# Performance work log

Hardware: AMD Instinct MI355X
Metric: run time of the kernel (lower is better)

The kernel has to match this reference:

```python
import jax, jax.numpy as jnp
import numpy as np

N_NODES = 50000
N_EDGES = 1600000
IN_DIM = 128
HEADS = 8
OUT_C = 16  # per-head channels; HEADS*OUT_C == IN_DIM -> residual active
NEG_SLOPE = 0.2
BN_EPS = 1e-5


def setup_inputs() -> dict:
    key = jax.random.key(0)
    ks = jax.random.split(key, 8)
    x = jax.random.normal(ks[0], (N_NODES, IN_DIM), dtype=jnp.float32)
    edge_index = jax.random.randint(ks[1], (2, N_EDGES), 0, N_NODES, dtype=jnp.int64)
    # GATConv params (PyG: shared lin for src/dst on single-tensor input)
    W = jax.random.normal(ks[2], (IN_DIM, HEADS * OUT_C), dtype=jnp.float32) / np.sqrt(IN_DIM)
    att_src = jax.random.normal(ks[3], (HEADS, OUT_C), dtype=jnp.float32) / np.sqrt(OUT_C)
    att_dst = jax.random.normal(ks[4], (HEADS, OUT_C), dtype=jnp.float32) / np.sqrt(OUT_C)
    bias = jnp.zeros((HEADS * OUT_C,), dtype=jnp.float32)
    # BatchNorm1d affine params
    gamma = jnp.ones((HEADS * OUT_C,), dtype=jnp.float32)
    beta = jnp.zeros((HEADS * OUT_C,), dtype=jnp.float32)
    return {"x": x, "edge_index": edge_index, "W": W, "att_src": att_src,
            "att_dst": att_dst, "bias": bias, "gamma": gamma, "beta": beta}


def reference(x, edge_index, W, att_src, att_dst, bias, gamma, beta):
    N = x.shape[0]
    H, C = att_src.shape
    src, dst = edge_index[0], edge_index[1]

    xl = (x @ W).reshape(N, H, C)                      # [N,H,C]
    a_src = jnp.sum(xl * att_src[None], axis=-1)       # [N,H]
    a_dst = jnp.sum(xl * att_dst[None], axis=-1)       # [N,H]

    e = jax.nn.leaky_relu(a_src[src] + a_dst[dst], NEG_SLOPE)  # [E,H]
    # segment softmax over incoming edges of each dst node
    m = jax.ops.segment_max(e, dst, num_segments=N)    # [N,H], -inf for empty
    m = jnp.where(jnp.isfinite(m), m, 0.0)
    ex = jnp.exp(e - m[dst])                           # [E,H]
    denom = jax.ops.segment_sum(ex, dst, num_segments=N)
    alpha = ex / (denom[dst] + 1e-16)                  # [E,H]

    out = jax.ops.segment_sum(alpha[:, :, None] * xl[src], dst, num_segments=N)  # [N,H,C]
    h = out.reshape(N, H * C) + bias

    # BatchNorm1d (training mode: batch statistics, biased variance)
    mean = jnp.mean(h, axis=0)
    var = jnp.mean((h - mean) ** 2, axis=0)
    h = (h - mean) * jax.lax.rsqrt(var + BN_EPS) * gamma + beta

    h = jax.nn.relu(h)
    return x + h  # residual (in_dim == H*C)
```

## Files before the change

kernel.cpp:

```cpp
#include <hip/hip_runtime.h>
#include <hip/hip_fp16.h>
#include <math.h>

#define N_NODES 50000
#define N_EDGES 1600000
#define DIM 128
#define HEADS 8
#define NEG_SLOPE 0.2f
#define BN_EPS 1e-5f

typedef _Float16 f16x8 __attribute__((ext_vector_type(8)));
typedef float f32x4 __attribute__((ext_vector_type(4)));

__global__ void k_wprep(const float* __restrict__ W, __half* __restrict__ Wh) {
    const int tid = blockIdx.x * 256 + threadIdx.x;
    const int g = tid >> 6;
    const int lane = tid & 63;
    const int nt = g >> 2, kt = g & 3;
    const int q = lane >> 4, n = lane & 15;
    #pragma unroll
    for (int j = 0; j < 8; ++j)
        Wh[(size_t)(g * 64 + lane) * 8 + j] =
            __float2half(W[(kt * 32 + q * 8 + j) * DIM + nt * 16 + n]);
}

__global__ __launch_bounds__(256) void k_lin(const float* __restrict__ x,
                      const __half* __restrict__ Wh, const float* __restrict__ att_s,
                      const float* __restrict__ att_d, __half* __restrict__ xlh,
                      float* __restrict__ a_src, float* __restrict__ a_dst) {
    const int wave = threadIdx.x >> 6;
    const int lane = threadIdx.x & 63;
    const int q = lane >> 4, n = lane & 15;
    const int nb = (blockIdx.x * 4 + wave) * 16;

    const int rowA = min(nb + n, N_NODES - 1);
    const float* xr = x + (size_t)rowA * DIM;
    f16x8 a[4];
    #pragma unroll
    for (int kt = 0; kt < 4; ++kt) {
        const float4 p0 = *(const float4*)(xr + kt * 32 + q * 8);
        const float4 p1 = *(const float4*)(xr + kt * 32 + q * 8 + 4);
        a[kt][0] = (_Float16)p0.x; a[kt][1] = (_Float16)p0.y;
        a[kt][2] = (_Float16)p0.z; a[kt][3] = (_Float16)p0.w;
        a[kt][4] = (_Float16)p1.x; a[kt][5] = (_Float16)p1.y;
        a[kt][6] = (_Float16)p1.z; a[kt][7] = (_Float16)p1.w;
    }

    f32x4 acc[8];
    #pragma unroll
    for (int nt = 0; nt < 8; ++nt) acc[nt] = (f32x4){0.f, 0.f, 0.f, 0.f};

    const f16x8* wb = (const f16x8*)Wh;
    #pragma unroll
    for (int nt = 0; nt < 8; ++nt) {
        #pragma unroll
        for (int kt = 0; kt < 4; ++kt) {
            const f16x8 b = wb[(nt * 4 + kt) * 64 + lane];
            acc[nt] = __builtin_amdgcn_mfma_f32_16x16x32_f16(a[kt], b, acc[nt], 0, 0, 0);
        }
    }

    const int r0 = nb + q * 4;
    #pragma unroll
    for (int nt = 0; nt < 8; ++nt) {
        const float as = att_s[nt * 16 + n];
        const float ad = att_d[nt * 16 + n];
        #pragma unroll
        for (int r = 0; r < 4; ++r) {
            const int row = r0 + r;
            const float v = acc[nt][r];
            float s = v * as;
            float d = v * ad;
            #pragma unroll
            for (int off = 8; off; off >>= 1) {
                s += __shfl_xor(s, off, 16);
                d += __shfl_xor(d, off, 16);
            }
            if (row < N_NODES) {
                xlh[(size_t)row * DIM + nt * 16 + n] = __float2half(v);
                if (n == 0) {
                    a_src[row * HEADS + nt] = s;
                    a_dst[row * HEADS + nt] = d;
                }
            }
        }
    }
}

#define SCAN_B 256
#define NBUCK 196
#define SEGCAP 12288
#define CHUNK 8192
#define NB_A ((N_EDGES + CHUNK - 1) / CHUNK)

__global__ __launch_bounds__(256) void k_binA(const int* __restrict__ ei,
                                              int* __restrict__ bcur,
                                              unsigned int* __restrict__ pairs) {
    __shared__ int hist[NBUCK], excl[NBUCK], gbase[NBUCK], cnt2[NBUCK];
    __shared__ int sc[SCAN_B];
    __shared__ unsigned int buf[CHUNK];
    const int t = threadIdx.x;
    const int base = blockIdx.x * CHUNK;
    const int cnt = min(CHUNK, N_EDGES - base);

    for (int j = t; j < NBUCK; j += 256) { hist[j] = 0; cnt2[j] = 0; }
    __syncthreads();
    for (int i = t; i < cnt; i += 256)
        atomicAdd(&hist[ei[N_EDGES + base + i] >> 8], 1);
    __syncthreads();
    sc[t] = (t < NBUCK) ? hist[t] : 0;
    __syncthreads();
    for (int d = 1; d < SCAN_B; d <<= 1) {
        const int xo = (t >= d) ? sc[t - d] : 0;
        __syncthreads();
        sc[t] += xo;
        __syncthreads();
    }
    if (t < NBUCK) {
        excl[t] = sc[t] - hist[t];
        gbase[t] = t * SEGCAP + atomicAdd(&bcur[t], hist[t]);
    }
    __syncthreads();
    for (int i = t; i < cnt; i += 256) {
        const int s = ei[base + i];
        const int d = ei[N_EDGES + base + i];
        const int b = d >> 8;
        const int r = atomicAdd(&cnt2[b], 1);
        buf[excl[b] + r] = (unsigned int)s | ((unsigned int)(d & 255) << 16)
                         | ((unsigned int)b << 24);
    }
    __syncthreads();
    for (int i = t; i < cnt; i += 256) {
        const unsigned int u = buf[i];
        const int b = u >> 24;
        pairs[gbase[b] + (i - excl[b])] = u & 0xFFFFFF;
    }
}

__global__ __launch_bounds__(512) void k_binB(const unsigned int* __restrict__ pairs,
                                              const int* __restrict__ bcur,
                                              unsigned short* __restrict__ csr,
                                              int2* __restrict__ nrange) {
    __shared__ int hist[256], excl[256], cnt2[256];
    __shared__ unsigned short out[SEGCAP];
    const int t = threadIdx.x;
    const int b = blockIdx.x;
    const int lo = b * SEGCAP;
    const int cnt = bcur[b];

    if (t < 256) { hist[t] = 0; cnt2[t] = 0; }
    __syncthreads();
    for (int i = t; i < cnt; i += 512)
        atomicAdd(&hist[pairs[lo + i] >> 16], 1);
    __syncthreads();
    if (t < 256) excl[t] = hist[t];
    __syncthreads();
    for (int d = 1; d < 256; d <<= 1) {
        int xo = 0;
        if (t < 256 && t >= d) xo = excl[t - d];
        __syncthreads();
        if (t < 256) excl[t] += xo;
        __syncthreads();
    }
    if (t < 256) excl[t] -= hist[t];
    __syncthreads();
    for (int i = t; i < cnt; i += 512) {
        const unsigned int u = pairs[lo + i];
        const int dl = u >> 16;
        const int r = atomicAdd(&cnt2[dl], 1);
        out[excl[dl] + r] = (unsigned short)(u & 0xFFFF);
    }
    __syncthreads();
    for (int i = t; i < cnt; i += 512)
        csr[2 * lo + i] = out[i];
    if (t < 256) {
        const int node = (b << 8) + t;
        if (node < N_NODES) {
            int2 rg;
            rg.x = 2 * lo + excl[t];
            rg.y = rg.x + hist[t];
            nrange[node] = rg;
        }
    }
}

__global__ void k_aggr2(const int2* __restrict__ nrange, const unsigned short* __restrict__ csr,
                        const float* __restrict__ a_src, const float* __restrict__ a_dst,
                        const __half* __restrict__ xlh, float* __restrict__ y) {
    const int d = blockIdx.x * 4 + (threadIdx.x >> 6);
    const int lane = threadIdx.x & 63;
    const int c2 = lane << 1;
    const int h = lane >> 3;
    const int2 rg = nrange[d];
    const int lo = rg.x, hi = rg.y;
    const float ad = a_dst[d * HEADS + h];
    float acc0 = 0.f, acc1 = 0.f, dsum = 0.f;
    int i = lo;
    for (; i + 8 <= hi; i += 8) {
        int s[8];
        float e[8];
        __half2 xv[8];
        #pragma unroll
        for (int j = 0; j < 8; ++j) s[j] = csr[i + j];
        #pragma unroll
        for (int j = 0; j < 8; ++j) e[j] = a_src[s[j] * HEADS + h] + ad;
        #pragma unroll
        for (int j = 0; j < 8; ++j)
            xv[j] = *(const __half2*)(xlh + (size_t)s[j] * DIM + c2);
        #pragma unroll
        for (int j = 0; j < 8; ++j) {
            const float w = __expf(fmaxf(e[j], NEG_SLOPE * e[j]));
            const float2 f = __half22float2(xv[j]);
            acc0 = fmaf(w, f.x, acc0);
            acc1 = fmaf(w, f.y, acc1);
            dsum += w;
        }
    }
    for (; i < hi; ++i) {
        const int s = csr[i];
        const float e = a_src[s * HEADS + h] + ad;
        const __half2 xv = *(const __half2*)(xlh + (size_t)s * DIM + c2);
        const float w = __expf(fmaxf(e, NEG_SLOPE * e));
        const float2 f = __half22float2(xv);
        acc0 = fmaf(w, f.x, acc0); acc1 = fmaf(w, f.y, acc1); dsum += w;
    }
    const float inv = 1.f / (dsum + 1e-16f);
    float2 o; o.x = acc0 * inv; o.y = acc1 * inv;
    *(float2*)(y + (size_t)d * DIM + c2) = o;
}

__global__ void k_stats(const float* __restrict__ y, const float* __restrict__ bias,
                        float* __restrict__ sums, float* __restrict__ sumsq) {
    const int c = threadIdx.x;
    const float b = bias[c];
    float s = 0.f, ss = 0.f;
    for (int n = blockIdx.x; n < N_NODES; n += gridDim.x) {
        const float h = y[n * DIM + c] + b;
        s += h;
        ss += h * h;
    }
    atomicAdd(sums + c, s);
    atomicAdd(sumsq + c, ss);
}

__global__ void k_statfin(const float* __restrict__ sums, const float* __restrict__ sumsq,
                          const float* __restrict__ gamma, const float* __restrict__ beta,
                          const float* __restrict__ bias, float* __restrict__ scale,
                          float* __restrict__ shift) {
    const int c = threadIdx.x;
    const float inv_n = 1.f / (float)N_NODES;
    const float mean = sums[c] * inv_n;
    const float var = sumsq[c] * inv_n - mean * mean;
    const float sc = rsqrtf(var + BN_EPS) * gamma[c];
    scale[c] = sc;
    shift[c] = beta[c] + (bias[c] - mean) * sc;
}

__global__ void k_final(float* __restrict__ y, const float* __restrict__ x,
                        const float* __restrict__ scale, const float* __restrict__ shift) {
    const int q = blockIdx.x * blockDim.x + threadIdx.x;
    const int cq = q & (DIM / 4 - 1);
    float4 v = ((const float4*)y)[q];
    const float4 xv = ((const float4*)x)[q];
    const float4 sc = ((const float4*)scale)[cq];
    const float4 sh = ((const float4*)shift)[cq];
    v.x = xv.x + fmaxf(v.x * sc.x + sh.x, 0.f);
    v.y = xv.y + fmaxf(v.y * sc.y + sh.y, 0.f);
    v.z = xv.z + fmaxf(v.z * sc.z + sh.z, 0.f);
    v.w = xv.w + fmaxf(v.w * sc.w + sh.w, 0.f);
    ((float4*)y)[q] = v;
}

extern "C" void kernel_launch(void* const* d_in, const int* in_sizes, int n_in,
                              void* d_out, int out_size, void* d_ws, size_t ws_size,
                              hipStream_t stream) {
    const float* x     = (const float*)d_in[0];
    const int*   ei    = (const int*)  d_in[1];
    const float* W     = (const float*)d_in[2];
    const float* att_s = (const float*)d_in[3];
    const float* att_d = (const float*)d_in[4];
    const float* bias  = (const float*)d_in[5];
    const float* gamma = (const float*)d_in[6];
    const float* beta  = (const float*)d_in[7];
    float* y = (float*)d_out;

    __half* xlh  = (__half*)d_ws;
    float* a_src = (float*)(xlh + (size_t)N_NODES * DIM);
    float* a_dst = a_src + (size_t)N_NODES * HEADS;
    float* sums  = a_dst + (size_t)N_NODES * HEADS;
    float* sumsq = sums  + DIM;
    float* scale = sumsq + DIM;
    float* shift = scale + DIM;
    int*   bcur  = (int*)(shift + DIM);
    int2*  nrange = (int2*)(bcur + 256);
    __half* Wh   = (__half*)(nrange + N_NODES);
    unsigned int* pairs = (unsigned int*)(Wh + 16384);
    unsigned short* csr = (unsigned short*)pairs;

    hipMemsetAsync(sums, 0, (4 * DIM + 256) * sizeof(float), stream);

    k_wprep<<<8, 256, 0, stream>>>(W, Wh);
    k_lin<<<(N_NODES + 63) / 64, 256, 0, stream>>>(x, Wh, att_s, att_d, xlh, a_src, a_dst);
    k_binA<<<NB_A, 256, 0, stream>>>(ei, bcur, pairs);
    k_binB<<<NBUCK, 512, 0, stream>>>(pairs, bcur, csr, nrange);
    k_aggr2<<<N_NODES / 4, 256, 0, stream>>>(nrange, csr, a_src, a_dst, xlh, y);
    k_stats<<<512, DIM, 0, stream>>>(y, bias, sums, sumsq);
    k_statfin<<<1, DIM, 0, stream>>>(sums, sumsq, gamma, beta, bias, scale, shift);
    k_final<<<(size_t)N_NODES * DIM / 4 / 256, 256, 0, stream>>>(y, x, scale, shift);
}
```

Before: 259.3 us.

## Fuse BN stats into aggregation, parallelize edge weights, vectorize binning, drop memset

The aggregation kernel now handles 16 nodes per wave. Each wave computes the edge attention weights for 16 edges in parallel across lanes and broadcasts them with shuffles, instead of every lane recomputing the exp for each edge. Batch-norm sum and sum-of-squares are accumulated inside the aggregation kernel through shared-memory atomics, which removes the separate stats pass that re-read y. The binning kernel reads edge indices as int4 vectors, and the memset is folded into the weight-prep kernel. The risks are lower occupancy and fewer blocks in aggregation (about 782), plus more shuffle traffic.

Result: faster. 253.9 us (-2.1%).

```diff
diff --git a/kernel.cpp b/kernel.cpp
--- a/kernel.cpp
+++ b/kernel.cpp
@@ -12,8 +12,13 @@
 typedef _Float16 f16x8 __attribute__((ext_vector_type(8)));
 typedef float f32x4 __attribute__((ext_vector_type(4)));
 
-__global__ void k_wprep(const float* __restrict__ W, __half* __restrict__ Wh) {
-    const int tid = blockIdx.x * 256 + threadIdx.x;
+__global__ void k_wprep(const float* __restrict__ W, __half* __restrict__ Wh,
+                        int* __restrict__ bcur, float* __restrict__ gsums,
+                        float* __restrict__ gsumsq) {
+    const int t = threadIdx.x;
+    if (blockIdx.x == 0 && t < 256) bcur[t] = 0;
+    if (blockIdx.x == 1 && t < DIM) { gsums[t] = 0.f; gsumsq[t] = 0.f; }
+    const int tid = blockIdx.x * 256 + t;
     const int g = tid >> 6;
     const int lane = tid & 63;
     const int nt = g >> 2, kt = g & 3;
@@ -105,8 +110,13 @@
 
     for (int j = t; j < NBUCK; j += 256) { hist[j] = 0; cnt2[j] = 0; }
     __syncthreads();
-    for (int i = t; i < cnt; i += 256)
-        atomicAdd(&hist[ei[N_EDGES + base + i] >> 8], 1);
+    for (int i = t * 4; i < cnt; i += 1024) {
+        const int4 dv = *(const int4*)(ei + N_EDGES + base + i);
+        atomicAdd(&hist[dv.x >> 8], 1);
+        atomicAdd(&hist[dv.y >> 8], 1);
+        atomicAdd(&hist[dv.z >> 8], 1);
+        atomicAdd(&hist[dv.w >> 8], 1);
+    }
     __syncthreads();
     sc[t] = (t < NBUCK) ? hist[t] : 0;
     __syncthreads();
@@ -121,13 +131,18 @@
         gbase[t] = t * SEGCAP + atomicAdd(&bcur[t], hist[t]);
     }
     __syncthreads();
-    for (int i = t; i < cnt; i += 256) {
-        const int s = ei[base + i];
-        const int d = ei[N_EDGES + base + i];
-        const int b = d >> 8;
-        const int r = atomicAdd(&cnt2[b], 1);
-        buf[excl[b] + r] = (unsigned int)s | ((unsigned int)(d & 255) << 16)
-                         | ((unsigned int)b << 24);
+    for (int i = t * 4; i < cnt; i += 1024) {
+        const int4 sv = *(const int4*)(ei + base + i);
+        const int4 dv = *(const int4*)(ei + N_EDGES + base + i);
+        const int ss[4] = {sv.x, sv.y, sv.z, sv.w};
+        const int dd[4] = {dv.x, dv.y, dv.z, dv.w};
+        #pragma unroll
+        for (int k = 0; k < 4; ++k) {
+            const int b = dd[k] >> 8;
+            const int r = atomicAdd(&cnt2[b], 1);
+            buf[excl[b] + r] = (unsigned int)ss[k] | ((unsigned int)(dd[k] & 255) << 16)
+                             | ((unsigned int)b << 24);
+        }
     }
     __syncthreads();
     for (int i = t; i < cnt; i += 256) {
@@ -184,63 +199,87 @@
     }
 }
 
-__global__ void k_aggr2(const int2* __restrict__ nrange, const unsigned short* __restrict__ csr,
+__global__ __launch_bounds__(256) void k_aggr3(const int2* __restrict__ nrange,
+                        const unsigned short* __restrict__ csr,
                         const float* __restrict__ a_src, const float* __restrict__ a_dst,
-                        const __half* __restrict__ xlh, float* __restrict__ y) {
-    const int d = blockIdx.x * 4 + (threadIdx.x >> 6);
-    const int lane = threadIdx.x & 63;
+                        const __half* __restrict__ xlh, const float* __restrict__ bias,
+                        float* __restrict__ y, float* __restrict__ gsums,
+                        float* __restrict__ gsumsq) {
+    __shared__ float ch_s[DIM], ch_ss[DIM];
+    const int t = threadIdx.x;
+    const int wave = t >> 6, lane = t & 63;
+    const int je = lane & 7;
+    const int h = lane >> 3;
     const int c2 = lane << 1;
-    const int h = lane >> 3;
-    const int2 rg = nrange[d];
-    const int lo = rg.x, hi = rg.y;
-    const float ad = a_dst[d * HEADS + h];
-    float acc0 = 0.f, acc1 = 0.f, dsum = 0.f;
-    int i = lo;
-    for (; i + 8 <= hi; i += 8) {
-        int s[8];
-        float e[8];
-        __half2 xv[8];
+    const int wbase = lane & 56;
+
+    if (t < DIM) { ch_s[t] = 0.f; ch_ss[t] = 0.f; }
+    __syncthreads();
+
+    const float b0 = bias[c2], b1 = bias[c2 + 1];
+    float ps0 = 0.f, pss0 = 0.f, ps1 = 0.f, pss1 = 0.f;
+
+    const int nb = (blockIdx.x * 4 + wave) * 16;
+    for (int ii = 0; ii < 16; ++ii) {
+        const int d = nb + ii;
+        if (d >= N_NODES) break;
+        const int2 rg = nrange[d];
+        const int lo = rg.x, hi = rg.y;
+        const float ad = a_dst[d * HEADS + h];
+        float acc0 = 0.f, acc1 = 0.f, dpart = 0.f;
+        for (int i = lo; i < hi; i += 16) {
+            int s0 = 0, s1 = 0;
+            float w0 = 0.f, w1 = 0.f;
+            if (i + je < hi) {
+                s0 = csr[i + je];
+                float e = a_src[s0 * HEADS + h] + ad;
+                e = fmaxf(e, NEG_SLOPE * e);
+                w0 = __expf(e);
+            }
+            if (i + 8 + je < hi) {
+                s1 = csr[i + 8 + je];
+                float e = a_src[s1 * HEADS + h] + ad;
+                e = fmaxf(e, NEG_SLOPE * e);
+                w1 = __expf(e);
+            }
+            dpart += w0 + w1;
+            int sb[16];
+            #pragma unroll
+            for (int j = 0; j < 8; ++j) sb[j] = __shfl(s0, j);
+            #pragma unroll
+            for (int j = 0; j < 8; ++j) sb[8 + j] = __shfl(s1, j);
+            __half2 xv[16];
+            #pragma unroll
+            for (int j = 0; j < 16; ++j)
+                xv[j] = *(const __half2*)(xlh + (size_t)sb[j] * DIM + c2);
+            #pragma unroll
+            for (int j = 0; j < 8; ++j) {
+                const float w = __shfl(w0, wbase | j);
+                const float2 f = __half22float2(xv[j]);
+                acc0 = fmaf(w, f.x, acc0); acc1 = fmaf(w, f.y, acc1);
+            }
+            #pragma unroll
+            for (int j = 0; j < 8; ++j) {
+                const float w = __shfl(w1, wbase | j);
+                const float2 f = __half22float2(xv[8 + j]);
+                acc0 = fmaf(w, f.x, acc0); acc1 = fmaf(w, f.y, acc1);
+            }
+        }
         #pragma unroll
-        for (int j = 0; j < 8; ++j) s[j] = csr[i + j];
-        #pragma unroll
-        for (int j = 0; j < 8; ++j) e[j] = a_src[s[j] * HEADS + h] + ad;
-        #pragma unroll
-        for (int j = 0; j < 8; ++j)
-            xv[j] = *(const __half2*)(xlh + (size_t)s[j] * DIM + c2);
-        #pragma unroll
-        for (int j = 0; j < 8; ++j) {
-            const float w = __expf(fmaxf(e[j], NEG_SLOPE * e[j]));
-            const float2 f = __half22float2(xv[j]);
-            acc0 = fmaf(w, f.x, acc0);
-            acc1 = fmaf(w, f.y, acc1);
-            dsum += w;
-        }
-    }
-    for (; i < hi; ++i) {
-        const int s = csr[i];
-        const float e = a_src[s * HEADS + h] + ad;
-        const __half2 xv = *(const __half2*)(xlh + (size_t)s * DIM + c2);
-        const float w = __expf(fmaxf(e, NEG_SLOPE * e));
-        const float2 f = __half22float2(xv);
-        acc0 = fmaf(w, f.x, acc0); acc1 = fmaf(w, f.y, acc1); dsum += w;
-    }
-    const float inv = 1.f / (dsum + 1e-16f);
-    float2 o; o.x = acc0 * inv; o.y = acc1 * inv;
-    *(float2*)(y + (size_t)d * DIM + c2) = o;
-}
-
-__global__ void k_stats(const float* __restrict__ y, const float* __restrict__ bias,
-                        float* __restrict__ sums, float* __restrict__ sumsq) {
-    const int c = threadIdx.x;
-    const float b = bias[c];
-    float s = 0.f, ss = 0.f;
-    for (int n = blockIdx.x; n < N_NODES; n += gridDim.x) {
-        const float h = y[n * DIM + c] + b;
-        s += h;
-        ss += h * h;
-    }
-    atomicAdd(sums + c, s);
-    atomicAdd(sumsq + c, ss);
+        for (int off = 1; off < 8; off <<= 1) dpart += __shfl_xor(dpart, off);
+        const float inv = 1.f / (dpart + 1e-16f);
+        const float o0 = acc0 * inv, o1 = acc1 * inv;
+        float2 o; o.x = o0; o.y = o1;
+        *(float2*)(y + (size_t)d * DIM + c2) = o;
+        const float h0 = o0 + b0, h1 = o1 + b1;
+        ps0 += h0; pss0 += h0 * h0;
+        ps1 += h1; pss1 += h1 * h1;
+    }
+    atomicAdd(&ch_s[c2], ps0);      atomicAdd(&ch_s[c2 + 1], ps1);
+    atomicAdd(&ch_ss[c2], pss0);    atomicAdd(&ch_ss[c2 + 1], pss1);
+    __syncthreads();
+    if (t < DIM) atomicAdd(&gsums[t], ch_s[t]);
+    else atomicAdd(&gsumsq[t - DIM], ch_ss[t - DIM]);
 }
 
 __global__ void k_statfin(const float* __restrict__ sums, const float* __restrict__ sumsq,
@@ -297,14 +336,12 @@
     unsigned int* pairs = (unsigned int*)(Wh + 16384);
     unsigned short* csr = (unsigned short*)pairs;
 
-    hipMemsetAsync(sums, 0, (4 * DIM + 256) * sizeof(float), stream);
-
-    k_wprep<<<8, 256, 0, stream>>>(W, Wh);
+    k_wprep<<<8, 256, 0, stream>>>(W, Wh, bcur, sums, sumsq);
     k_lin<<<(N_NODES + 63) / 64, 256, 0, stream>>>(x, Wh, att_s, att_d, xlh, a_src, a_dst);
     k_binA<<<NB_A, 256, 0, stream>>>(ei, bcur, pairs);
     k_binB<<<NBUCK, 512, 0, stream>>>(pairs, bcur, csr, nrange);
-    k_aggr2<<<N_NODES / 4, 256, 0, stream>>>(nrange, csr, a_src, a_dst, xlh, y);
-    k_stats<<<512, DIM, 0, stream>>>(y, bias, sums, sumsq);
+    k_aggr3<<<(N_NODES + 63) / 64, 256, 0, stream>>>(nrange, csr, a_src, a_dst, xlh,
+                                                     bias, y, sums, sumsq);
     k_statfin<<<1, DIM, 0, stream>>>(sums, sumsq, gamma, beta, bias, scale, shift);
     k_final<<<(size_t)N_NODES * DIM / 4 / 256, 256, 0, stream>>>(y, x, scale, shift);
 }
```
